# Kernel optimization log

Hardware: AMD Instinct MI355X
Metric: run time of the kernel (lower is better)

Reference implementation:

```python
import jax, jax.numpy as jnp
import numpy as np

BS, SL, H, DH = 2, 2048, 32, 128
STRIDE = 16
NUM_PAGES = BS * (SL // STRIDE)  # 256, distinct page per block
PAGE_DIM = 1 * 2 * STRIDE * H * DH  # blocks * partitions * stride * kv_heads * head_dim


def setup_inputs() -> dict:
    key = jax.random.key(0)
    k1, k2, k3 = jax.random.split(key, 3)
    xq = jax.random.normal(k1, (BS, SL, H, DH), dtype=jnp.float32)
    xk = jax.random.normal(k2, (BS, SL, H, DH), dtype=jnp.float32)
    xv = jax.random.normal(k3, (BS, SL, H, DH), dtype=jnp.float32)
    cache_state = jnp.zeros((NUM_PAGES, PAGE_DIM), dtype=jnp.float32)
    seq_block_ids = jnp.arange(BS * (SL // STRIDE), dtype=jnp.int64 if jax.config.jax_enable_x64 else jnp.int32).reshape(BS, SL // STRIDE)
    return {"xq": xq, "xk": xk, "xv": xv, "cache_state": cache_state, "seq_block_ids": seq_block_ids}


def reference(xq, xk, xv, cache_state, seq_block_ids):
    bs, sl, h, dh = xq.shape
    nb = sl // STRIDE  # blocks per sequence
    num_pages = cache_state.shape[0]

    # --- paged cache write (prefill path: start_positions is None) ---
    # page layout: [page, transformer_block(=1), partition(k=0,v=1), stride, head, head_dim]
    cache = cache_state.reshape(num_pages, 1, 2, STRIDE, h, dh)
    pids = seq_block_ids.reshape(-1)  # [bs*nb]
    k_blocks = xk.reshape(bs * nb, STRIDE, h, dh)
    v_blocks = xv.reshape(bs * nb, STRIDE, h, dh)
    cache = cache.at[pids, 0, 0].set(k_blocks)
    cache = cache.at[pids, 0, 1].set(v_blocks)
    new_cache_state = cache.reshape(cache_state.shape)

    # --- GQA repeat_kv: n_rep = head_count // head_count_kv = 1 -> no-op ---

    # --- SDPA, attn_mask=None, is_causal=False ---
    scale = 1.0 / np.sqrt(dh).astype(np.float32)
    scores = jnp.einsum("bqhd,bkhd->bhqk", xq, xk) * scale  # [bs, h, sl, sl]
    attn = jax.nn.softmax(scores, axis=-1)
    out = jnp.einsum("bhqk,bkhd->bqhd", attn, xv)
    attn_output = out.reshape(bs, sl, h * dh)
    return attn_output, new_cache_state
```

## Files before the change

kernel.cpp:

```cpp
#include <hip/hip_runtime.h>
#include <hip/hip_bf16.h>
#include <stdint.h>

#define BS 2
#define SL 2048
#define H 32
#define DH 128
#define ATT_ELEMS (BS*SL*H*DH)
#define KTILES (SL/64)
#define KT32 (SL/32)
#define QSCALE (0.08838834764831845f * 1.4426950408889634f)
#define MFIX 10.0f

typedef __attribute__((ext_vector_type(8))) short short8_t;
typedef __attribute__((ext_vector_type(16))) float f32x16_t;
typedef __attribute__((ext_vector_type(4))) unsigned int u32x4_t;
typedef __attribute__((ext_vector_type(2))) unsigned int u32x2_t;

union FragU { u32x4_t u; short8_t s; };

__device__ __forceinline__ unsigned short f2bf(float x){
    union { float f; unsigned int u; } v; v.f = x;
    unsigned int r = v.u + 0x7fffu + ((v.u >> 16) & 1u);
    return (unsigned short)(r >> 16);
}
__device__ __forceinline__ unsigned int pack2(float a, float b){
    return (unsigned int)f2bf(a) | ((unsigned int)f2bf(b) << 16);
}
__device__ __forceinline__ unsigned int cvtpk(float a, float b){
    unsigned int r;
    asm("v_cvt_pk_bf16_f32 %0, %1, %2" : "=v"(r) : "v"(a), "v"(b));
    return r;
}
__device__ __forceinline__ void gload16(const unsigned short* g, unsigned short* l){
    __builtin_amdgcn_global_load_lds(
        (const __attribute__((address_space(1))) void*)(const void*)g,
        (__attribute__((address_space(3))) void*)(void*)l, 16, 0, 0);
}

__global__ __launch_bounds__(256) void prep_kv_kernel(const float* __restrict__ xk,
                                                      const float* __restrict__ xv,
                                                      const int* __restrict__ pids,
                                                      unsigned short* __restrict__ kfr,
                                                      unsigned short* __restrict__ vfr,
                                                      float* __restrict__ out_cache,
                                                      int do_cache){
    __shared__ unsigned short tK[64*136];
    __shared__ unsigned short tV[64*136];
    int tile = blockIdx.x, h = blockIdx.y, b = blockIdx.z;
    int tid = threadIdx.x;
    size_t tb = ((size_t)((b*H + h)*KTILES + tile)) * 8192;
    int pg[4];
    #pragma unroll
    for (int j = 0; j < 4; ++j) pg[j] = pids[b*128 + tile*4 + j];

    #pragma unroll
    for (int i = 0; i < 8; ++i){
        int c = tid + 256*i;
        int row = c >> 5, f4 = c & 31;
        size_t gidx = ((size_t)((b*SL + tile*64 + row)*H + h))*DH + f4*4;
        float4 kx = *(const float4*)(xk + gidx);
        float4 vx = *(const float4*)(xv + gidx);
        u32x2_t kw; kw[0] = pack2(kx.x, kx.y); kw[1] = pack2(kx.z, kx.w);
        u32x2_t vw; vw[0] = pack2(vx.x, vx.y); vw[1] = pack2(vx.z, vx.w);
        *(u32x2_t*)(&tK[row*136 + f4*4]) = kw;
        *(u32x2_t*)(&tV[row*136 + f4*4]) = vw;
        if (do_cache){
            size_t cb = (size_t)pg[row>>4]*131072 + (size_t)(row&15)*4096 + h*128 + f4*4;
            *(float4*)(out_cache + cb)         = kx;
            *(float4*)(out_cache + cb + 65536) = vx;
        }
    }
    __syncthreads();
    #pragma unroll
    for (int i = 0; i < 4; ++i){
        int c = tid + 256*i;
        int sub = c >> 9, c2 = c & 511;
        int fi = c2 >> 6, l = c2 & 63;
        int key = sub*32 + (l & 31);
        int d0  = fi*16 + (l >> 5)*8;
        u32x4_t w = *(const u32x4_t*)(&tK[key*136 + d0]);
        *(u32x4_t*)(&kfr[tb + (size_t)sub*4096 + (size_t)c2*8]) = w;
    }
    #pragma unroll
    for (int i = 0; i < 4; ++i){
        int c = tid + 256*i;
        int sub = c >> 9, c2 = c & 511;
        int fi = c2 >> 6, l = c2 & 63;
        int d  = (fi >> 1)*32 + (l & 31);
        int k0 = sub*32 + (fi & 1)*16 + (l >> 5)*8;
        u32x4_t u;
        #pragma unroll
        for (int w = 0; w < 4; ++w)
            u[w] = (unsigned)tV[(k0+2*w)*136 + d] | ((unsigned)tV[(k0+2*w+1)*136 + d] << 16);
        *(u32x4_t*)(&vfr[tb + (size_t)sub*4096 + (size_t)c2*8]) = u;
    }
}

__global__ __launch_bounds__(256) void cache_scatter_kernel(const float* __restrict__ xk,
                                                            const float* __restrict__ xv,
                                                            const int* __restrict__ pids,
                                                            float* __restrict__ out_cache){
    int sb = blockIdx.x >> 1, part = blockIdx.x & 1;
    int page = pids[sb];
    const float4* s4 = (const float4*)((part ? xv : xk) + (size_t)sb * 65536);
    float4* d4 = (float4*)(out_cache + (size_t)page * 131072 + (size_t)part * 65536);
    int base = blockIdx.y * 2048 + threadIdx.x;
    #pragma unroll
    for (int i = 0; i < 8; ++i) d4[base + i*256] = s4[base + i*256];
}

__global__ __launch_bounds__(256, 2) void attn_kernel(const float* __restrict__ xq,
                                                      const unsigned short* __restrict__ kfr,
                                                      const unsigned short* __restrict__ vfr,
                                                      float* __restrict__ out){
    __shared__ unsigned short smem[2*8192];

    const int tid  = threadIdx.x;
    const int lane = tid & 63;
    const int wave = tid >> 6;
    const int l31  = lane & 31;
    const int hi   = lane >> 5;

    int lin = blockIdx.x;
    int swz = (lin & 7)*64 + (lin >> 3);
    const int qblk = swz & 7;
    const int h    = (swz >> 3) & 31;
    const int b    = swz >> 8;
    const int qbase = qblk*256 + wave*64;

    short8_t qf0[8], qf1[8];
    #pragma unroll
    for (int qb = 0; qb < 2; ++qb){
        const float* qptr = xq + ((size_t)((b*SL + qbase + qb*32 + l31)*H + h))*DH + hi*8;
        #pragma unroll
        for (int f = 0; f < 8; ++f){
            float4 a = *(const float4*)(qptr + f*16);
            float4 c = *(const float4*)(qptr + f*16 + 4);
            FragU w;
            w.u[0] = pack2(a.x*QSCALE, a.y*QSCALE);
            w.u[1] = pack2(a.z*QSCALE, a.w*QSCALE);
            w.u[2] = pack2(c.x*QSCALE, c.y*QSCALE);
            w.u[3] = pack2(c.z*QSCALE, c.w*QSCALE);
            if (qb == 0) qf0[f] = w.s; else qf1[f] = w.s;
        }
    }

    f32x16_t acc0[4], acc1[4];
    #pragma unroll
    for (int d = 0; d < 4; ++d)
        #pragma unroll
        for (int r = 0; r < 16; ++r){ acc0[d][r] = 0.f; acc1[d][r] = 0.f; }
    float l0 = 0.f, l1 = 0.f;

    const size_t bh = (size_t)(b*H + h) * ((size_t)KT32*4096);
    const unsigned short* kg = kfr + bh;
    const unsigned short* vg = vfr + bh;

    #pragma unroll
    for (int i = 0; i < 2; ++i){
        int ch = wave*2 + i;
        gload16(kg + ch*512 + lane*8, smem + ch*512);
        gload16(vg + ch*512 + lane*8, smem + 4096 + ch*512);
    }
    asm volatile("s_waitcnt vmcnt(0)" ::: "memory");
    __builtin_amdgcn_s_barrier();
    asm volatile("" ::: "memory");

    #pragma unroll 1
    for (int t = 0; t < KT32; ++t){
        const int p = t & 1;
        const unsigned short* Kc = smem + p*8192;
        const unsigned short* Vc = Kc + 4096;

        if (t + 1 < KT32){
            const unsigned short* kn = kg + (size_t)(t+1)*4096;
            const unsigned short* vn = vg + (size_t)(t+1)*4096;
            unsigned short* Kn = smem + (p^1)*8192;
            #pragma unroll
            for (int i = 0; i < 2; ++i){
                int ch = wave*2 + i;
                gload16(kn + ch*512 + lane*8, Kn + ch*512);
                gload16(vn + ch*512 + lane*8, Kn + 4096 + ch*512);
            }
        }
        __builtin_amdgcn_sched_barrier(0);

        f32x16_t s0, s1;
        #pragma unroll
        for (int r = 0; r < 16; ++r){ s0[r] = -MFIX; s1[r] = -MFIX; }
        __builtin_amdgcn_s_setprio(1);
        #pragma unroll
        for (int f = 0; f < 8; ++f){
            FragU kf; kf.u = *(const u32x4_t*)(&Kc[f*512 + lane*8]);
            s0 = __builtin_amdgcn_mfma_f32_32x32x16_bf16(kf.s, qf0[f], s0, 0, 0, 0);
            s1 = __builtin_amdgcn_mfma_f32_32x32x16_bf16(kf.s, qf1[f], s1, 0, 0, 0);
        }
        __builtin_amdgcn_s_setprio(0);

        FragU pf0[2], pf1[2];
        #define PSLICE(SV, PF, KS, RB, LR)                                                  \
        {                                                                                   \
            float e0 = __builtin_amdgcn_exp2f(SV[RB+0]);                                    \
            float e1 = __builtin_amdgcn_exp2f(SV[RB+1]);                                    \
            float e2 = __builtin_amdgcn_exp2f(SV[RB+2]);                                    \
            float e3 = __builtin_amdgcn_exp2f(SV[RB+3]);                                    \
            float e4 = __builtin_amdgcn_exp2f(SV[RB+4]);                                    \
            float e5 = __builtin_amdgcn_exp2f(SV[RB+5]);                                    \
            float e6 = __builtin_amdgcn_exp2f(SV[RB+6]);                                    \
            float e7 = __builtin_amdgcn_exp2f(SV[RB+7]);                                    \
            LR += ((e0+e1)+(e2+e3)) + ((e4+e5)+(e6+e7));                                    \
            unsigned a  = cvtpk(e0,e1), bq = cvtpk(e2,e3);                                  \
            unsigned cq = cvtpk(e4,e5), dq = cvtpk(e6,e7);                                  \
            unsigned y0 = hi ? a : cq,  y1 = hi ? bq : dq;                                  \
            unsigned r0 = __shfl_xor(y0, 32, 64);                                           \
            unsigned r1 = __shfl_xor(y1, 32, 64);                                           \
            PF[KS].u[0] = hi ? r0 : a;  PF[KS].u[1] = hi ? r1 : bq;                         \
            PF[KS].u[2] = hi ? cq : r0; PF[KS].u[3] = hi ? dq : r1;                         \
        }
        PSLICE(s0, pf0, 0, 0, l0)
        PSLICE(s0, pf0, 1, 8, l0)
        PSLICE(s1, pf1, 0, 0, l1)
        PSLICE(s1, pf1, 1, 8, l1)
        #undef PSLICE

        __builtin_amdgcn_s_setprio(1);
        #pragma unroll
        for (int dblk = 0; dblk < 4; ++dblk){
            #pragma unroll
            for (int ks = 0; ks < 2; ++ks){
                FragU vb;
                vb.u = *(const u32x4_t*)(&Vc[(dblk*2 + ks)*512 + lane*8]);
                acc0[dblk] = __builtin_amdgcn_mfma_f32_32x32x16_bf16(pf0[ks].s, vb.s, acc0[dblk], 0, 0, 0);
                acc1[dblk] = __builtin_amdgcn_mfma_f32_32x32x16_bf16(pf1[ks].s, vb.s, acc1[dblk], 0, 0, 0);
            }
        }
        __builtin_amdgcn_s_setprio(0);

        if (t + 1 < KT32){
            asm volatile("s_waitcnt vmcnt(0)" ::: "memory");
            __builtin_amdgcn_s_barrier();
            asm volatile("" ::: "memory");
        }
    }

    l0 += __shfl_xor(l0, 32, 64);
    l1 += __shfl_xor(l1, 32, 64);

    #pragma unroll
    for (int qb = 0; qb < 2; ++qb){
        float linv = 1.f / (qb ? l1 : l0);
        float lr[16];
        #pragma unroll
        for (int r = 0; r < 16; ++r)
            lr[r] = __shfl(linv, (r&3) + 8*(r>>2) + 4*hi, 64);
        int q0 = qbase + qb*32;
        #pragma unroll
        for (int dblk = 0; dblk < 4; ++dblk){
            #pragma unroll
            for (int r = 0; r < 16; ++r){
                int q = q0 + (r&3) + 8*(r>>2) + 4*hi;
                float v = (qb ? acc1[dblk][r] : acc0[dblk][r]) * lr[r];
                out[(size_t)(b*SL + q)*(H*DH) + h*DH + dblk*32 + l31] = v;
            }
        }
    }
}

extern "C" void kernel_launch(void* const* d_in, const int* in_sizes, int n_in,
                              void* d_out, int out_size, void* d_ws, size_t ws_size,
                              hipStream_t stream) {
    const float* xq = (const float*)d_in[0];
    const float* xk = (const float*)d_in[1];
    const float* xv = (const float*)d_in[2];
    const int* pids = (const int*)d_in[4];

    float* out_attn  = (float*)d_out;
    float* out_cache = out_attn + (size_t)ATT_ELEMS;

    const size_t frag_elems = (size_t)BS*H*KTILES*8192;
    const size_t need       = 2*frag_elems*sizeof(unsigned short);

    if (ws_size >= need){
        unsigned short* kfr = (unsigned short*)d_ws;
        unsigned short* vfr = kfr + frag_elems;
        prep_kv_kernel<<<dim3(KTILES, H, BS), 256, 0, stream>>>(xk, xv, pids, kfr, vfr, out_cache, 1);
        attn_kernel<<<dim3(BS*H*(SL/256)), 256, 0, stream>>>(xq, kfr, vfr, out_attn);
    } else {
        unsigned short* vfr = (unsigned short*)out_cache;
        unsigned short* kfr = vfr + frag_elems;
        prep_kv_kernel<<<dim3(KTILES, H, BS), 256, 0, stream>>>(xk, xv, pids, kfr, vfr, out_cache, 0);
        attn_kernel<<<dim3(BS*H*(SL/256)), 256, 0, stream>>>(xq, kfr, vfr, out_attn);
        cache_scatter_kernel<<<dim3(512, 8), 256, 0, stream>>>(xk, xv, pids, out_cache);
    }
}
```

Measured before the change: 214.5 us.

## Process 64-key tiles per iteration and interleave QK with PV across halves

The attention loop now stages 64 keys of K and V per iteration into a double-buffered LDS region twice as large, instead of 32. This halves the number of wait-and-barrier points per block. Inside each iteration the QK MFMAs for the second 32-key half are issued before the PV MFMAs of the first half, so the softmax exp and pack work can overlap with matrix work. The priority hints are dropped. LDS per block doubles to 64 KB, which may limit occupancy, and holding more live fragments raises register pressure.

```diff
diff --git a/kernel.cpp b/kernel.cpp
--- a/kernel.cpp
+++ b/kernel.cpp
@@ -8,7 +8,6 @@
 #define DH 128
 #define ATT_ELEMS (BS*SL*H*DH)
 #define KTILES (SL/64)
-#define KT32 (SL/32)
 #define QSCALE (0.08838834764831845f * 1.4426950408889634f)
 #define MFIX 10.0f
 
@@ -114,7 +113,7 @@
                                                       const unsigned short* __restrict__ kfr,
                                                       const unsigned short* __restrict__ vfr,
                                                       float* __restrict__ out){
-    __shared__ unsigned short smem[2*8192];
+    __shared__ unsigned short smem[2*16384];
 
     const int tid  = threadIdx.x;
     const int lane = tid & 63;
@@ -153,52 +152,52 @@
         for (int r = 0; r < 16; ++r){ acc0[d][r] = 0.f; acc1[d][r] = 0.f; }
     float l0 = 0.f, l1 = 0.f;
 
-    const size_t bh = (size_t)(b*H + h) * ((size_t)KT32*4096);
+    const size_t bh = (size_t)(b*H + h) * ((size_t)KTILES*8192);
     const unsigned short* kg = kfr + bh;
     const unsigned short* vg = vfr + bh;
 
     #pragma unroll
-    for (int i = 0; i < 2; ++i){
-        int ch = wave*2 + i;
+    for (int i = 0; i < 4; ++i){
+        int ch = wave*4 + i;
         gload16(kg + ch*512 + lane*8, smem + ch*512);
-        gload16(vg + ch*512 + lane*8, smem + 4096 + ch*512);
-    }
-    asm volatile("s_waitcnt vmcnt(0)" ::: "memory");
-    __builtin_amdgcn_s_barrier();
-    asm volatile("" ::: "memory");
+        gload16(vg + ch*512 + lane*8, smem + 8192 + ch*512);
+    }
 
     #pragma unroll 1
-    for (int t = 0; t < KT32; ++t){
-        const int p = t & 1;
-        const unsigned short* Kc = smem + p*8192;
-        const unsigned short* Vc = Kc + 4096;
-
-        if (t + 1 < KT32){
-            const unsigned short* kn = kg + (size_t)(t+1)*4096;
-            const unsigned short* vn = vg + (size_t)(t+1)*4096;
-            unsigned short* Kn = smem + (p^1)*8192;
+    for (int t = 0; t < KTILES; ++t){
+        const unsigned short* Kc = smem + (t & 1)*16384;
+        const unsigned short* Vc = Kc + 8192;
+
+        asm volatile("s_waitcnt vmcnt(0)" ::: "memory");
+        __builtin_amdgcn_s_barrier();
+        asm volatile("" ::: "memory");
+
+        if (t + 1 < KTILES){
+            const unsigned short* kn = kg + (size_t)(t+1)*8192;
+            const unsigned short* vn = vg + (size_t)(t+1)*8192;
+            unsigned short* Kn = smem + ((t+1) & 1)*16384;
             #pragma unroll
-            for (int i = 0; i < 2; ++i){
-                int ch = wave*2 + i;
+            for (int i = 0; i < 4; ++i){
+                int ch = wave*4 + i;
                 gload16(kn + ch*512 + lane*8, Kn + ch*512);
-                gload16(vn + ch*512 + lane*8, Kn + 4096 + ch*512);
+                gload16(vn + ch*512 + lane*8, Kn + 8192 + ch*512);
             }
         }
         __builtin_amdgcn_sched_barrier(0);
 
-        f32x16_t s0, s1;
-        #pragma unroll
-        for (int r = 0; r < 16; ++r){ s0[r] = -MFIX; s1[r] = -MFIX; }
-        __builtin_amdgcn_s_setprio(1);
-        #pragma unroll
-        for (int f = 0; f < 8; ++f){
-            FragU kf; kf.u = *(const u32x4_t*)(&Kc[f*512 + lane*8]);
-            s0 = __builtin_amdgcn_mfma_f32_32x32x16_bf16(kf.s, qf0[f], s0, 0, 0, 0);
-            s1 = __builtin_amdgcn_mfma_f32_32x32x16_bf16(kf.s, qf1[f], s1, 0, 0, 0);
-        }
-        __builtin_amdgcn_s_setprio(0);
-
-        FragU pf0[2], pf1[2];
+        FragU pfA0[2], pfA1[2], pfB0[2], pfB1[2];
+
+        #define QK_HALF(OFS, S0, S1)                                                        \
+        {                                                                                   \
+            _Pragma("unroll")                                                               \
+            for (int r = 0; r < 16; ++r){ S0[r] = -MFIX; S1[r] = -MFIX; }                   \
+            _Pragma("unroll")                                                               \
+            for (int f = 0; f < 8; ++f){                                                    \
+                FragU kf; kf.u = *(const u32x4_t*)(&Kc[(OFS) + f*512 + lane*8]);            \
+                S0 = __builtin_amdgcn_mfma_f32_32x32x16_bf16(kf.s, qf0[f], S0, 0, 0, 0);    \
+                S1 = __builtin_amdgcn_mfma_f32_32x32x16_bf16(kf.s, qf1[f], S1, 0, 0, 0);    \
+            }                                                                               \
+        }
         #define PSLICE(SV, PF, KS, RB, LR)                                                  \
         {                                                                                   \
             float e0 = __builtin_amdgcn_exp2f(SV[RB+0]);                                    \
@@ -218,30 +217,37 @@
             PF[KS].u[0] = hi ? r0 : a;  PF[KS].u[1] = hi ? r1 : bq;                         \
             PF[KS].u[2] = hi ? cq : r0; PF[KS].u[3] = hi ? dq : r1;                         \
         }
-        PSLICE(s0, pf0, 0, 0, l0)
-        PSLICE(s0, pf0, 1, 8, l0)
-        PSLICE(s1, pf1, 0, 0, l1)
-        PSLICE(s1, pf1, 1, 8, l1)
+        #define PV_HALF(VOFS, PF0, PF1)                                                     \
+        {                                                                                   \
+            _Pragma("unroll")                                                               \
+            for (int dblk = 0; dblk < 4; ++dblk){                                           \
+                _Pragma("unroll")                                                           \
+                for (int ks = 0; ks < 2; ++ks){                                             \
+                    FragU vb;                                                               \
+                    vb.u = *(const u32x4_t*)(&Vc[(VOFS) + (dblk*2 + ks)*512 + lane*8]);     \
+                    acc0[dblk] = __builtin_amdgcn_mfma_f32_32x32x16_bf16((PF0)[ks].s, vb.s, acc0[dblk], 0, 0, 0); \
+                    acc1[dblk] = __builtin_amdgcn_mfma_f32_32x32x16_bf16((PF1)[ks].s, vb.s, acc1[dblk], 0, 0, 0); \
+                }                                                                           \
+            }                                                                               \
+        }
+
+        f32x16_t s0, s1;
+        QK_HALF(0, s0, s1)
+        PSLICE(s0, pfA0, 0, 0, l0)
+        PSLICE(s1, pfA1, 0, 0, l1)
+        PSLICE(s0, pfA0, 1, 8, l0)
+        PSLICE(s1, pfA1, 1, 8, l1)
+        QK_HALF(4096, s0, s1)
+        PV_HALF(0, pfA0, pfA1)
+        PSLICE(s0, pfB0, 0, 0, l0)
+        PSLICE(s1, pfB1, 0, 0, l1)
+        PSLICE(s0, pfB0, 1, 8, l0)
+        PSLICE(s1, pfB1, 1, 8, l1)
+        PV_HALF(4096, pfB0, pfB1)
+
+        #undef QK_HALF
         #undef PSLICE
-
-        __builtin_amdgcn_s_setprio(1);
-        #pragma unroll
-        for (int dblk = 0; dblk < 4; ++dblk){
-            #pragma unroll
-            for (int ks = 0; ks < 2; ++ks){
-                FragU vb;
-                vb.u = *(const u32x4_t*)(&Vc[(dblk*2 + ks)*512 + lane*8]);
-                acc0[dblk] = __builtin_amdgcn_mfma_f32_32x32x16_bf16(pf0[ks].s, vb.s, acc0[dblk], 0, 0, 0);
-                acc1[dblk] = __builtin_amdgcn_mfma_f32_32x32x16_bf16(pf1[ks].s, vb.s, acc1[dblk], 0, 0, 0);
-            }
-        }
-        __builtin_amdgcn_s_setprio(0);
-
-        if (t + 1 < KT32){
-            asm volatile("s_waitcnt vmcnt(0)" ::: "memory");
-            __builtin_amdgcn_s_barrier();
-            asm volatile("" ::: "memory");
-        }
+        #undef PV_HALF
     }
 
     l0 += __shfl_xor(l0, 32, 64);
```

Result: slower. 296.7 us (+38.3%).
